# Kernel optimization log

Measured on AMD Instinct MI355X. Metric: run time of the kernel, lower is better.

## Reference

```python
import jax, jax.numpy as jnp
import numpy as np

N_NODES = 50000
N_EDGES = 800000
NFEAT, NHID, NCLASS = 512, 128, 40
PN_SCALE = 1.0


def spmm(edge_row, edge_col, edge_val, h):
    # sparse [N,N] @ dense [N,F]: out[r] += val * h[c] for each edge (r, c)
    msgs = edge_val[:, None] * h[edge_col]  # [E, F]
    return jax.ops.segment_sum(msgs, edge_row, num_segments=N_NODES)


def pair_norm(x):
    # mode 'PN': center columns, scale by mean row norm
    x = x - x.mean(axis=0)
    rownorm_mean = jnp.sqrt(1e-6 + (x * x).sum(axis=1).mean())
    return PN_SCALE * x / rownorm_mean


def setup_inputs() -> dict:
    key = jax.random.key(0)
    ks = jax.random.split(key, 12)

    def uinit(k, shape, fan_out):
        stdv = 1.0 / np.sqrt(fan_out)
        return jax.random.uniform(k, shape, jnp.float32, -stdv, stdv)

    return {
        "x": jax.random.normal(ks[0], (N_NODES, NFEAT), jnp.float32),
        "edge_row": jax.random.randint(ks[1], (N_EDGES,), 0, N_NODES),
        "edge_col": jax.random.randint(ks[2], (N_EDGES,), 0, N_NODES),
        "edge_val": jax.random.uniform(ks[3], (N_EDGES,), jnp.float32),
        "W0": uinit(ks[4], (NFEAT, NHID), NHID),
        "b0": uinit(ks[5], (1, NHID), NHID),
        "W1": uinit(ks[6], (NHID, NHID), NHID),
        "b1": uinit(ks[7], (1, NHID), NHID),
        "W2": uinit(ks[8], (NHID, NHID), NHID),
        "b2": uinit(ks[9], (1, NHID), NHID),
        "W_out": uinit(ks[10], (NHID, NCLASS), NCLASS),
        "b_out": uinit(ks[11], (1, NCLASS), NCLASS),
    }


def reference(x, edge_row, edge_col, edge_val,
              W0, b0, W1, b1, W2, b2, W_out, b_out):
    # DeepGCN forward, eval mode (dropout p=0 is identity), residual=1 -> skip every layer
    x_old = 0.0
    for W, b in ((W0, b0), (W1, b1), (W2, b2)):
        h = x @ W                             # dense mm
        h = spmm(edge_row, edge_col, edge_val, h) + b  # sparse aggregate + bias
        h = pair_norm(h)
        h = jax.nn.relu(h)
        h = h + x_old                         # residual (x_old=0 on first layer)
        x_old = h
        x = h
    out = spmm(edge_row, edge_col, edge_val, x @ W_out) + b_out
    return out
```

## Files before the change

### kernel.cpp

```cpp
#include <hip/hip_runtime.h>
#include <hip/hip_bf16.h>
#include <math.h>

#define N_NODES 50000
#define N_EDGES 800000
#define NFEAT   512
#define NHID    128
#define NCLASS  40
#define NB_STATS 256
#define NPASS    8
#define ROWS_PER_PASS (N_NODES / NPASS)
#define NCB      8
#define CB_W     (N_NODES / NCB)
#define NCNT     (N_NODES * NCB)
#define SCAN_BLOCKS ((NCNT + 1023) / 1024)

typedef short bf16x8 __attribute__((ext_vector_type(8)));
typedef float f32x4  __attribute__((ext_vector_type(4)));

__device__ inline float bf2f(unsigned short u) {
    union { unsigned int i; float f; } x; x.i = ((unsigned int)u) << 16; return x.f;
}

__global__ void hist_kernel(const int* __restrict__ rows, const int* __restrict__ cols,
                            int* __restrict__ cnt, int n) {
    int i = blockIdx.x * blockDim.x + threadIdx.x;
    if (i < n) {
        int r = rows[i];
        int cb = cols[i] / CB_W;
        atomicAdd(&cnt[r * NCB + cb], 1);
    }
}

__global__ __launch_bounds__(1024) void scan_p1_kernel(const int* __restrict__ cnt,
                                                       int* __restrict__ bsum, int n) {
    int i = blockIdx.x * 1024 + threadIdx.x;
    int v = (i < n) ? cnt[i] : 0;
    __shared__ int sm[16];
    int lane = threadIdx.x & 63, w = threadIdx.x >> 6;
    #pragma unroll
    for (int off = 32; off > 0; off >>= 1) v += __shfl_xor(v, off, 64);
    if (lane == 0) sm[w] = v;
    __syncthreads();
    if (threadIdx.x == 0) {
        int s = 0;
        #pragma unroll
        for (int j = 0; j < 16; ++j) s += sm[j];
        bsum[blockIdx.x] = s;
    }
}

__global__ __launch_bounds__(512) void scan_p2_kernel(int* __restrict__ bsum, int nb) {
    __shared__ int wsum[8];
    int t = threadIdx.x;
    int lane = t & 63, w = t >> 6;
    int v = (t < nb) ? bsum[t] : 0;
    int x = v;
    #pragma unroll
    for (int off = 1; off < 64; off <<= 1) {
        int y = __shfl_up(x, off, 64);
        if (lane >= off) x += y;
    }
    if (lane == 63) wsum[w] = x;
    __syncthreads();
    int wbase = 0;
    for (int j = 0; j < w; ++j) wbase += wsum[j];
    if (t < nb) bsum[t] = wbase + x - v;
}

__global__ __launch_bounds__(1024) void scan_p3_kernel(const int* __restrict__ cnt,
                                                       const int* __restrict__ bsum,
                                                       int* __restrict__ bptr,
                                                       int* __restrict__ cursor, int n) {
    __shared__ int wsum[16];
    int b = blockIdx.x;
    int i = b * 1024 + threadIdx.x;
    int lane = threadIdx.x & 63, w = threadIdx.x >> 6;
    int v = (i < n) ? cnt[i] : 0;
    int x = v;
    #pragma unroll
    for (int off = 1; off < 64; off <<= 1) {
        int y = __shfl_up(x, off, 64);
        if (lane >= off) x += y;
    }
    if (lane == 63) wsum[w] = x;
    __syncthreads();
    int wbase = 0;
    for (int j = 0; j < w; ++j) wbase += wsum[j];
    int incl = bsum[b] + wbase + x;
    if (i < n) {
        bptr[i + 1] = incl;
        cursor[i] = incl - v;
    }
    if (i == 0) bptr[0] = 0;
}

__global__ void scatter_kernel(const int* __restrict__ rows, const int* __restrict__ cols,
                               const float* __restrict__ vals, int* __restrict__ cursor,
                               int2* __restrict__ csr_cv, int n, int blocksPerPass) {
    int p = blockIdx.x / blocksPerPass;
    int b = blockIdx.x % blocksPerPass;
    int i = b * 256 + threadIdx.x;
    if (i >= n) return;
    int r = rows[i];
    int lo = p * ROWS_PER_PASS;
    if (r < lo || r >= lo + ROWS_PER_PASS) return;
    int c = cols[i];
    int pos = atomicAdd(&cursor[r * NCB + c / CB_W], 1);
    csr_cv[pos] = make_int2(c, __float_as_int(vals[i]));
}

__global__ __launch_bounds__(256) void wt_cvt_all_kernel(const float* __restrict__ W0,
        const float* __restrict__ W1, const float* __restrict__ W2,
        const float* __restrict__ Wo, __hip_bfloat16* __restrict__ Wt0,
        __hip_bfloat16* __restrict__ Wt1, __hip_bfloat16* __restrict__ Wt2,
        __hip_bfloat16* __restrict__ Wot) {
    int i = blockIdx.x * blockDim.x + threadIdx.x;
    if (i < 65536) {
        int k = i >> 7, n = i & 127;
        Wt0[(size_t)n * 512 + k] = __float2bfloat16(W0[i]);
    } else if (i < 65536 + 16384) {
        int j = i - 65536; int k = j >> 7, n = j & 127;
        Wt1[(size_t)n * 128 + k] = __float2bfloat16(W1[j]);
    } else if (i < 65536 + 32768) {
        int j = i - 65536 - 16384; int k = j >> 7, n = j & 127;
        Wt2[(size_t)n * 128 + k] = __float2bfloat16(W2[j]);
    } else if (i < 65536 + 32768 + 8192) {
        int j = i - 65536 - 32768; int k = j >> 6, n = j & 63;
        float v = (n < NCLASS) ? Wo[k * NCLASS + n] : 0.f;
        Wot[(size_t)n * 128 + k] = __float2bfloat16(v);
    }
}

template<int BM, int BN, int K>
__global__ __launch_bounds__(256) void mfma_gemm(const __hip_bfloat16* __restrict__ Xb,
                                                 const __hip_bfloat16* __restrict__ Wt,
                                                 __hip_bfloat16* __restrict__ Ob, int M) {
    constexpr int BK  = 64;
    constexpr int LDK = 72;
    constexpr int WN  = BN / 64;
    __shared__ short As[BM * LDK];
    __shared__ short Bs[BN * LDK];
    int t = threadIdx.x;
    int lane = t & 63;
    int w = t >> 6;
    int wm = w / WN, wn = w % WN;
    int row0 = blockIdx.x * BM;
    int m0 = wm * 32, n0 = wn * 64;
    int l15 = lane & 15, quad = lane >> 4;

    f32x4 acc[2][4] = {};

    for (int k0 = 0; k0 < K; k0 += BK) {
        #pragma unroll
        for (int idx = t; idx < BM * 8; idx += 256) {
            int r = idx >> 3, c = idx & 7;
            uint4 v = make_uint4(0u, 0u, 0u, 0u);
            if (row0 + r < M)
                v = *(const uint4*)(Xb + (size_t)(row0 + r) * K + k0 + c * 8);
            *(uint4*)(As + r * LDK + c * 8) = v;
        }
        #pragma unroll
        for (int idx = t; idx < BN * 8; idx += 256) {
            int r = idx >> 3, c = idx & 7;
            uint4 v = *(const uint4*)(Wt + (size_t)r * K + k0 + c * 8);
            *(uint4*)(Bs + r * LDK + c * 8) = v;
        }
        __syncthreads();
        #pragma unroll
        for (int ks = 0; ks < 2; ++ks) {
            bf16x8 af[2], bfv[4];
            #pragma unroll
            for (int mt = 0; mt < 2; ++mt)
                af[mt] = *(const bf16x8*)(As + (m0 + mt * 16 + l15) * LDK + ks * 32 + quad * 8);
            #pragma unroll
            for (int nt = 0; nt < 4; ++nt)
                bfv[nt] = *(const bf16x8*)(Bs + (n0 + nt * 16 + l15) * LDK + ks * 32 + quad * 8);
            #pragma unroll
            for (int mt = 0; mt < 2; ++mt)
                #pragma unroll
                for (int nt = 0; nt < 4; ++nt)
                    acc[mt][nt] = __builtin_amdgcn_mfma_f32_16x16x32_bf16(
                        af[mt], bfv[nt], acc[mt][nt], 0, 0, 0);
        }
        __syncthreads();
    }
    #pragma unroll
    for (int mt = 0; mt < 2; ++mt) {
        #pragma unroll
        for (int reg = 0; reg < 4; ++reg) {
            int row = row0 + m0 + mt * 16 + quad * 4 + reg;
            if (row < M) {
                #pragma unroll
                for (int nt = 0; nt < 4; ++nt)
                    Ob[(size_t)row * BN + n0 + nt * 16 + l15] =
                        __float2bfloat16(acc[mt][nt][reg]);
            }
        }
    }
}

template<int BM, int BN, int K>
__global__ __launch_bounds__(256) void mfma_gemm_f32a(const float* __restrict__ Xg,
                                                      const __hip_bfloat16* __restrict__ Wt,
                                                      __hip_bfloat16* __restrict__ Ob, int M) {
    constexpr int BK  = 64;
    constexpr int LDK = 72;
    constexpr int WN  = BN / 64;
    __shared__ short As[BM * LDK];
    __shared__ short Bs[BN * LDK];
    int t = threadIdx.x;
    int lane = t & 63;
    int w = t >> 6;
    int wm = w / WN, wn = w % WN;
    int row0 = blockIdx.x * BM;
    int m0 = wm * 32, n0 = wn * 64;
    int l15 = lane & 15, quad = lane >> 4;

    f32x4 acc[2][4] = {};

    for (int k0 = 0; k0 < K; k0 += BK) {
        #pragma unroll
        for (int idx = t; idx < BM * 16; idx += 256) {
            int r = idx >> 4, c = idx & 15;
            float4 v = make_float4(0.f, 0.f, 0.f, 0.f);
            if (row0 + r < M)
                v = *(const float4*)(Xg + (size_t)(row0 + r) * K + k0 + c * 4);
            __hip_bfloat16 o[4] = {__float2bfloat16(v.x), __float2bfloat16(v.y),
                                   __float2bfloat16(v.z), __float2bfloat16(v.w)};
            *(short4*)(As + r * LDK + c * 4) = *(short4*)o;
        }
        #pragma unroll
        for (int idx = t; idx < BN * 8; idx += 256) {
            int r = idx >> 3, c = idx & 7;
            uint4 v = *(const uint4*)(Wt + (size_t)r * K + k0 + c * 8);
            *(uint4*)(Bs + r * LDK + c * 8) = v;
        }
        __syncthreads();
        #pragma unroll
        for (int ks = 0; ks < 2; ++ks) {
            bf16x8 af[2], bfv[4];
            #pragma unroll
            for (int mt = 0; mt < 2; ++mt)
                af[mt] = *(const bf16x8*)(As + (m0 + mt * 16 + l15) * LDK + ks * 32 + quad * 8);
            #pragma unroll
            for (int nt = 0; nt < 4; ++nt)
                bfv[nt] = *(const bf16x8*)(Bs + (n0 + nt * 16 + l15) * LDK + ks * 32 + quad * 8);
            #pragma unroll
            for (int mt = 0; mt < 2; ++mt)
                #pragma unroll
                for (int nt = 0; nt < 4; ++nt)
                    acc[mt][nt] = __builtin_amdgcn_mfma_f32_16x16x32_bf16(
                        af[mt], bfv[nt], acc[mt][nt], 0, 0, 0);
        }
        __syncthreads();
    }
    #pragma unroll
    for (int mt = 0; mt < 2; ++mt) {
        #pragma unroll
        for (int reg = 0; reg < 4; ++reg) {
            int row = row0 + m0 + mt * 16 + quad * 4 + reg;
            if (row < M) {
                #pragma unroll
                for (int nt = 0; nt < 4; ++nt)
                    Ob[(size_t)row * BN + n0 + nt * 16 + l15] =
                        __float2bfloat16(acc[mt][nt][reg]);
            }
        }
    }
}

__global__ __launch_bounds__(256) void spmm_bf16_kernel(const __hip_bfloat16* __restrict__ H,
                                                        const int* __restrict__ bptr,
                                                        const int2* __restrict__ cv,
                                                        const float* __restrict__ bias,
                                                        __hip_bfloat16* __restrict__ Bm,
                                                        int nrows) {
    int wid = (int)((blockIdx.x * blockDim.x + threadIdx.x) >> 6);
    wid = __builtin_amdgcn_readfirstlane(wid);
    int lane = threadIdx.x & 63;
    int h = lane >> 5;
    int sub = lane & 31;
    if (wid >= nrows) return;
    int s = bptr[wid * NCB];
    int e = bptr[wid * NCB + NCB];
    const ushort4* H4 = (const ushort4*)H;
    f32x4 acc = {0.f, 0.f, 0.f, 0.f};
    int i = s;
    for (; i + 7 < e; i += 8) {
        int2 c0 = cv[i],     c1 = cv[i + 1], c2 = cv[i + 2], c3 = cv[i + 3];
        int2 c4 = cv[i + 4], c5 = cv[i + 5], c6 = cv[i + 6], c7 = cv[i + 7];
        int   ka = h ? c4.x : c0.x;  float va = __int_as_float(h ? c4.y : c0.y);
        int   kb = h ? c5.x : c1.x;  float vb = __int_as_float(h ? c5.y : c1.y);
        int   kc = h ? c6.x : c2.x;  float vc = __int_as_float(h ? c6.y : c2.y);
        int   kd = h ? c7.x : c3.x;  float vd = __int_as_float(h ? c7.y : c3.y);
        ushort4 ga = H4[(size_t)ka * 32 + sub];
        ushort4 gb = H4[(size_t)kb * 32 + sub];
        ushort4 gc = H4[(size_t)kc * 32 + sub];
        ushort4 gd = H4[(size_t)kd * 32 + sub];
        acc[0] = fmaf(va, bf2f(ga.x), acc[0]); acc[1] = fmaf(va, bf2f(ga.y), acc[1]);
        acc[2] = fmaf(va, bf2f(ga.z), acc[2]); acc[3] = fmaf(va, bf2f(ga.w), acc[3]);
        acc[0] = fmaf(vb, bf2f(gb.x), acc[0]); acc[1] = fmaf(vb, bf2f(gb.y), acc[1]);
        acc[2] = fmaf(vb, bf2f(gb.z), acc[2]); acc[3] = fmaf(vb, bf2f(gb.w), acc[3]);
        acc[0] = fmaf(vc, bf2f(gc.x), acc[0]); acc[1] = fmaf(vc, bf2f(gc.y), acc[1]);
        acc[2] = fmaf(vc, bf2f(gc.z), acc[2]); acc[3] = fmaf(vc, bf2f(gc.w), acc[3]);
        acc[0] = fmaf(vd, bf2f(gd.x), acc[0]); acc[1] = fmaf(vd, bf2f(gd.y), acc[1]);
        acc[2] = fmaf(vd, bf2f(gd.z), acc[2]); acc[3] = fmaf(vd, bf2f(gd.w), acc[3]);
    }
    for (; i + 3 < e; i += 4) {
        int2 c0 = cv[i], c1 = cv[i + 1], c2 = cv[i + 2], c3 = cv[i + 3];
        int   ka = h ? c2.x : c0.x;  float va = __int_as_float(h ? c2.y : c0.y);
        int   kb = h ? c3.x : c1.x;  float vb = __int_as_float(h ? c3.y : c1.y);
        ushort4 ga = H4[(size_t)ka * 32 + sub];
        ushort4 gb = H4[(size_t)kb * 32 + sub];
        acc[0] = fmaf(va, bf2f(ga.x), acc[0]); acc[1] = fmaf(va, bf2f(ga.y), acc[1]);
        acc[2] = fmaf(va, bf2f(ga.z), acc[2]); acc[3] = fmaf(va, bf2f(ga.w), acc[3]);
        acc[0] = fmaf(vb, bf2f(gb.x), acc[0]); acc[1] = fmaf(vb, bf2f(gb.y), acc[1]);
        acc[2] = fmaf(vb, bf2f(gb.z), acc[2]); acc[3] = fmaf(vb, bf2f(gb.w), acc[3]);
    }
    for (; i < e; ++i) {
        int2 c = cv[i];
        if (h == 0) {
            float v = __int_as_float(c.y);
            ushort4 g = H4[(size_t)c.x * 32 + sub];
            acc[0] = fmaf(v, bf2f(g.x), acc[0]); acc[1] = fmaf(v, bf2f(g.y), acc[1]);
            acc[2] = fmaf(v, bf2f(g.z), acc[2]); acc[3] = fmaf(v, bf2f(g.w), acc[3]);
        }
    }
    #pragma unroll
    for (int c = 0; c < 4; ++c) acc[c] += __shfl_xor(acc[c], 32);
    if (h == 0) {
        float4 b4 = *(const float4*)(bias + 4 * sub);
        __hip_bfloat16 o[4] = {__float2bfloat16(acc[0] + b4.x), __float2bfloat16(acc[1] + b4.y),
                               __float2bfloat16(acc[2] + b4.z), __float2bfloat16(acc[3] + b4.w)};
        *(ushort4*)(Bm + (size_t)wid * 128 + 4 * sub) = *(ushort4*)o;
    }
}

__global__ __launch_bounds__(256) void stats_kernel(const __hip_bfloat16* __restrict__ B,
                                                    float* __restrict__ partials, int n2) {
    int tid = blockIdx.x * blockDim.x + threadIdx.x;
    int stride = NB_STATS * 256;
    const __hip_bfloat162* B2 = (const __hip_bfloat162*)B;
    float cs0 = 0.f, cs1 = 0.f, sq = 0.f;
    for (int j = tid; j < n2; j += stride) {
        __hip_bfloat162 h = B2[j];
        float a = __bfloat162float(h.x), b = __bfloat162float(h.y);
        cs0 += a; cs1 += b;
        sq = fmaf(a, a, sq); sq = fmaf(b, b, sq);
    }
    __shared__ float s0[256], s1[256], ss[256];
    int t = threadIdx.x;
    s0[t] = cs0; s1[t] = cs1; ss[t] = sq;
    __syncthreads();
    if (t < 64) {
        float a = s0[t] + s0[t + 64] + s0[t + 128] + s0[t + 192];
        float b = s1[t] + s1[t + 64] + s1[t + 128] + s1[t + 192];
        float* pb = partials + (size_t)blockIdx.x * 132;
        pb[2 * t] = a;
        pb[2 * t + 1] = b;
    }
    __syncthreads();
    for (int off = 128; off > 0; off >>= 1) {
        if (t < off) ss[t] += ss[t + off];
        __syncthreads();
    }
    if (t == 0) partials[(size_t)blockIdx.x * 132 + 128] = ss[0];
}

__global__ void finalize_stats_kernel(const float* __restrict__ partials,
                                      float* __restrict__ stats, int nrows) {
    int t = threadIdx.x;
    float cs = 0.f;
    for (int b = 0; b < NB_STATS; ++b) cs += partials[(size_t)b * 132 + t];
    float mu = cs / (float)nrows;
    __shared__ float smu2[128];
    __shared__ float ssq[128];
    float sq = 0.f;
    for (int b = t; b < NB_STATS; b += 128) sq += partials[(size_t)b * 132 + 128];
    smu2[t] = mu * mu;
    ssq[t] = sq;
    __syncthreads();
    for (int off = 64; off > 0; off >>= 1) {
        if (t < off) { smu2[t] += smu2[t + off]; ssq[t] += ssq[t + off]; }
        __syncthreads();
    }
    if (t == 0) {
        float ms = ssq[0] / (float)nrows - smu2[0];
        stats[129] = 1.0f / sqrtf(1e-6f + ms);
    }
    stats[t] = mu;
}

__global__ __launch_bounds__(256) void pn_apply_kernel(const __hip_bfloat16* __restrict__ B,
                                                       const float* __restrict__ stats,
                                                       __hip_bfloat16* __restrict__ Xb,
                                                       int n4, int addResid) {
    int i = blockIdx.x * blockDim.x + threadIdx.x;
    if (i >= n4) return;
    ushort4 bv = *(const ushort4*)(B + (size_t)i * 4);
    __hip_bfloat16* bb = (__hip_bfloat16*)&bv;
    int c4 = (i << 2) & 127;
    float s = stats[129];
    float4 m = ((const float4*)stats)[c4 >> 2];
    float r0 = 0.f, r1 = 0.f, r2 = 0.f, r3 = 0.f;
    if (addResid) {
        ushort4 rv = *(const ushort4*)(Xb + (size_t)i * 4);
        __hip_bfloat16* rb = (__hip_bfloat16*)&rv;
        r0 = __bfloat162float(rb[0]); r1 = __bfloat162float(rb[1]);
        r2 = __bfloat162float(rb[2]); r3 = __bfloat162float(rb[3]);
    }
    __hip_bfloat16 o[4];
    o[0] = __float2bfloat16(fmaxf((__bfloat162float(bb[0]) - m.x) * s, 0.f) + r0);
    o[1] = __float2bfloat16(fmaxf((__bfloat162float(bb[1]) - m.y) * s, 0.f) + r1);
    o[2] = __float2bfloat16(fmaxf((__bfloat162float(bb[2]) - m.z) * s, 0.f) + r2);
    o[3] = __float2bfloat16(fmaxf((__bfloat162float(bb[3]) - m.w) * s, 0.f) + r3);
    *(ushort4*)(Xb + (size_t)i * 4) = *(ushort4*)o;
}

__global__ __launch_bounds__(256) void spmm_out_kernel(const __hip_bfloat16* __restrict__ G,
                                                       const int* __restrict__ bptr,
                                                       const int2* __restrict__ cv,
                                                       const float* __restrict__ bias,
                                                       float* __restrict__ out, int nrows) {
    int wid = (int)((blockIdx.x * blockDim.x + threadIdx.x) >> 6);
    wid = __builtin_amdgcn_readfirstlane(wid);
    int lane = threadIdx.x & 63;
    int h = lane >> 5;
    int sub = lane & 31;
    if (wid >= nrows) return;
    int s = bptr[wid * NCB];
    int e = bptr[wid * NCB + NCB];
    const __hip_bfloat162* G2 = (const __hip_bfloat162*)G;
    float a0 = 0.f, a1 = 0.f;
    int i = s;
    for (; i + 7 < e; i += 8) {
        int2 c0 = cv[i],     c1 = cv[i + 1], c2 = cv[i + 2], c3 = cv[i + 3];
        int2 c4 = cv[i + 4], c5 = cv[i + 5], c6 = cv[i + 6], c7 = cv[i + 7];
        int   ka = h ? c4.x : c0.x;  float va = __int_as_float(h ? c4.y : c0.y);
        int   kb = h ? c5.x : c1.x;  float vb = __int_as_float(h ? c5.y : c1.y);
        int   kc = h ? c6.x : c2.x;  float vc = __int_as_float(h ? c6.y : c2.y);
        int   kd = h ? c7.x : c3.x;  float vd = __int_as_float(h ? c7.y : c3.y);
        __hip_bfloat162 ga = G2[(size_t)ka * 32 + sub];
        __hip_bfloat162 gb = G2[(size_t)kb * 32 + sub];
        __hip_bfloat162 gc = G2[(size_t)kc * 32 + sub];
        __hip_bfloat162 gd = G2[(size_t)kd * 32 + sub];
        a0 = fmaf(va, __bfloat162float(ga.x), a0); a1 = fmaf(va, __bfloat162float(ga.y), a1);
        a0 = fmaf(vb, __bfloat162float(gb.x), a0); a1 = fmaf(vb, __bfloat162float(gb.y), a1);
        a0 = fmaf(vc, __bfloat162float(gc.x), a0); a1 = fmaf(vc, __bfloat162float(gc.y), a1);
        a0 = fmaf(vd, __bfloat162float(gd.x), a0); a1 = fmaf(vd, __bfloat162float(gd.y), a1);
    }
    for (; i + 3 < e; i += 4) {
        int2 c0 = cv[i], c1 = cv[i + 1], c2 = cv[i + 2], c3 = cv[i + 3];
        int   ka = h ? c2.x : c0.x;  float va = __int_as_float(h ? c2.y : c0.y);
        int   kb = h ? c3.x : c1.x;  float vb = __int_as_float(h ? c3.y : c1.y);
        __hip_bfloat162 ga = G2[(size_t)ka * 32 + sub];
        __hip_bfloat162 gb = G2[(size_t)kb * 32 + sub];
        a0 = fmaf(va, __bfloat162float(ga.x), a0); a1 = fmaf(va, __bfloat162float(ga.y), a1);
        a0 = fmaf(vb, __bfloat162float(gb.x), a0); a1 = fmaf(vb, __bfloat162float(gb.y), a1);
    }
    for (; i < e; ++i) {
        int2 c = cv[i];
        if (h == 0) {
            float v = __int_as_float(c.y);
            __hip_bfloat162 g = G2[(size_t)c.x * 32 + sub];
            a0 = fmaf(v, __bfloat162float(g.x), a0);
            a1 = fmaf(v, __bfloat162float(g.y), a1);
        }
    }
    a0 += __shfl_xor(a0, 32);
    a1 += __shfl_xor(a1, 32);
    if (h == 0 && sub < NCLASS / 2) {
        float2 b2 = *(const float2*)(bias + 2 * sub);
        float2 o = make_float2(a0 + b2.x, a1 + b2.y);
        *(float2*)(out + (size_t)wid * NCLASS + 2 * sub) = o;
    }
}

extern "C" void kernel_launch(void* const* d_in, const int* in_sizes, int n_in,
                              void* d_out, int out_size, void* d_ws, size_t ws_size,
                              hipStream_t stream) {
    const float* x        = (const float*)d_in[0];
    const int*   edge_row = (const int*)  d_in[1];
    const int*   edge_col = (const int*)  d_in[2];
    const float* edge_val = (const float*)d_in[3];
    const float* W0 = (const float*)d_in[4];
    const float* b0 = (const float*)d_in[5];
    const float* W1 = (const float*)d_in[6];
    const float* b1 = (const float*)d_in[7];
    const float* W2 = (const float*)d_in[8];
    const float* b2 = (const float*)d_in[9];
    const float* W_out = (const float*)d_in[10];
    const float* b_out = (const float*)d_in[11];
    float* out = (float*)d_out;

    const size_t NH = (size_t)N_NODES * NHID;

    char* p = (char*)d_ws;
    __hip_bfloat16* Xb   = (__hip_bfloat16*)p;  p += NH * 2;
    __hip_bfloat16* A_bf = (__hip_bfloat16*)p;  p += NH * 2;
    __hip_bfloat16* Bm   = (__hip_bfloat16*)p;  p += NH * 2;
    __hip_bfloat16* Wt0 = (__hip_bfloat16*)p;   p += (size_t)128 * 512 * 2;
    __hip_bfloat16* Wt1 = (__hip_bfloat16*)p;   p += (size_t)128 * 128 * 2;
    __hip_bfloat16* Wt2 = (__hip_bfloat16*)p;   p += (size_t)128 * 128 * 2;
    __hip_bfloat16* Wot = (__hip_bfloat16*)p;   p += (size_t)64 * 128 * 2;
    float* stats    = (float*)p;                p += 132 * 4;
    float* partials = (float*)p;                p += (size_t)NB_STATS * 132 * 4;
    int* cnt      = (int*)p;                    p += (size_t)NCNT * 4;
    int* bptr     = (int*)p;                    p += (size_t)(NCNT + 1) * 4 + 4;
    int* cursor   = (int*)p;                    p += (size_t)NCNT * 4;
    int* bsum     = (int*)p;                    p += (size_t)SCAN_BLOCKS * 4 + 4;
    int2* csr_cv  = (int2*)p;                   p += (size_t)N_EDGES * 8;

    const int EB = (N_EDGES + 255) / 256;
    const int SPMM_GRID = (N_NODES + 3) / 4;
    const int PN_GRID = (int)(NH / 4 + 255) / 256;

    wt_cvt_all_kernel<<<(65536 + 32768 + 8192 + 255) / 256, 256, 0, stream>>>(
        W0, W1, W2, W_out, Wt0, Wt1, Wt2, Wot);

    hipMemsetAsync(cnt, 0, NCNT * sizeof(int), stream);
    hist_kernel<<<EB, 256, 0, stream>>>(edge_row, edge_col, cnt, N_EDGES);
    scan_p1_kernel<<<SCAN_BLOCKS, 1024, 0, stream>>>(cnt, bsum, NCNT);
    scan_p2_kernel<<<1, 512, 0, stream>>>(bsum, SCAN_BLOCKS);
    scan_p3_kernel<<<SCAN_BLOCKS, 1024, 0, stream>>>(cnt, bsum, bptr, cursor, NCNT);
    scatter_kernel<<<EB * NPASS, 256, 0, stream>>>(edge_row, edge_col, edge_val, cursor,
                                                   csr_cv, N_EDGES, EB);

    mfma_gemm_f32a<64, 128, 512><<<(N_NODES + 63) / 64, 256, 0, stream>>>(x, Wt0, A_bf, N_NODES);
    spmm_bf16_kernel<<<SPMM_GRID, 256, 0, stream>>>(A_bf, bptr, csr_cv, b0, Bm, N_NODES);
    stats_kernel<<<NB_STATS, 256, 0, stream>>>(Bm, partials, (int)(NH / 2));
    finalize_stats_kernel<<<1, 128, 0, stream>>>(partials, stats, N_NODES);
    pn_apply_kernel<<<PN_GRID, 256, 0, stream>>>(Bm, stats, Xb, (int)(NH / 4), 0);

    const __hip_bfloat16* Wts[2] = {Wt1, Wt2};
    const float* bs[2] = {b1, b2};
    for (int l = 0; l < 2; ++l) {
        mfma_gemm<64, 128, 128><<<(N_NODES + 63) / 64, 256, 0, stream>>>(Xb, Wts[l], A_bf, N_NODES);
        spmm_bf16_kernel<<<SPMM_GRID, 256, 0, stream>>>(A_bf, bptr, csr_cv, bs[l], Bm, N_NODES);
        stats_kernel<<<NB_STATS, 256, 0, stream>>>(Bm, partials, (int)(NH / 2));
        finalize_stats_kernel<<<1, 128, 0, stream>>>(partials, stats, N_NODES);
        pn_apply_kernel<<<PN_GRID, 256, 0, stream>>>(Bm, stats, Xb, (int)(NH / 4), 1);
    }

    mfma_gemm<128, 64, 128><<<(N_NODES + 127) / 128, 256, 0, stream>>>(Xb, Wot, A_bf, N_NODES);
    spmm_out_kernel<<<SPMM_GRID, 256, 0, stream>>>(A_bf, bptr, csr_cv, b_out,
                                                   out, N_NODES);
}
```

Baseline: 496.6 us.

## Fuse PairNorm stats into SpMM and PairNorm apply into next GEMM

Column sums and the sum of squares are now accumulated inside the SpMM kernel: a persistent grid-stride loop reduces into shared memory and then into global stats with atomics. The separate stats, finalize and apply kernels are removed. Normalization, ReLU and the residual add are applied while the next GEMM loads its A tile, and the result is written back to Xb only where later layers need it. This removes several full passes over the hidden activations and many launches, at the cost of global float atomics (non-deterministic summation order) and a persistent SpMM grid that may balance load differently. NPASS for the scatter kernel also changes from 8 to 4.

```diff
diff --git a/kernel.cpp b/kernel.cpp
--- a/kernel.cpp
+++ b/kernel.cpp
@@ -7,13 +7,14 @@
 #define NFEAT   512
 #define NHID    128
 #define NCLASS  40
-#define NB_STATS 256
-#define NPASS    8
+#define NPASS    4
 #define ROWS_PER_PASS (N_NODES / NPASS)
 #define NCB      8
 #define CB_W     (N_NODES / NCB)
 #define NCNT     (N_NODES * NCB)
 #define SCAN_BLOCKS ((NCNT + 1023) / 1024)
+#define NSTAT    132
+#define SPMM_BLOCKS 1024
 
 typedef short bf16x8 __attribute__((ext_vector_type(8)));
 typedef float f32x4  __attribute__((ext_vector_type(4)));
@@ -133,15 +134,17 @@
 }
 
 template<int BM, int BN, int K>
-__global__ __launch_bounds__(256) void mfma_gemm(const __hip_bfloat16* __restrict__ Xb,
-                                                 const __hip_bfloat16* __restrict__ Wt,
-                                                 __hip_bfloat16* __restrict__ Ob, int M) {
+__global__ __launch_bounds__(256) void mfma_gemm_f32a(const float* __restrict__ Xg,
+                                                      const __hip_bfloat16* __restrict__ Wt,
+                                                      __hip_bfloat16* __restrict__ Ob,
+                                                      float* __restrict__ stats_out, int M) {
     constexpr int BK  = 64;
     constexpr int LDK = 72;
     constexpr int WN  = BN / 64;
     __shared__ short As[BM * LDK];
     __shared__ short Bs[BN * LDK];
     int t = threadIdx.x;
+    if (blockIdx.x == 0 && t < NSTAT) stats_out[t] = 0.f;
     int lane = t & 63;
     int w = t >> 6;
     int wm = w / WN, wn = w % WN;
@@ -153,12 +156,14 @@
 
     for (int k0 = 0; k0 < K; k0 += BK) {
         #pragma unroll
-        for (int idx = t; idx < BM * 8; idx += 256) {
-            int r = idx >> 3, c = idx & 7;
-            uint4 v = make_uint4(0u, 0u, 0u, 0u);
+        for (int idx = t; idx < BM * 16; idx += 256) {
+            int r = idx >> 4, c = idx & 15;
+            float4 v = make_float4(0.f, 0.f, 0.f, 0.f);
             if (row0 + r < M)
-                v = *(const uint4*)(Xb + (size_t)(row0 + r) * K + k0 + c * 8);
-            *(uint4*)(As + r * LDK + c * 8) = v;
+                v = *(const float4*)(Xg + (size_t)(row0 + r) * K + k0 + c * 4);
+            __hip_bfloat16 o[4] = {__float2bfloat16(v.x), __float2bfloat16(v.y),
+                                   __float2bfloat16(v.z), __float2bfloat16(v.w)};
+            *(short4*)(As + r * LDK + c * 4) = *(short4*)o;
         }
         #pragma unroll
         for (int idx = t; idx < BN * 8; idx += 256) {
@@ -200,16 +205,39 @@
     }
 }
 
-template<int BM, int BN, int K>
-__global__ __launch_bounds__(256) void mfma_gemm_f32a(const float* __restrict__ Xg,
-                                                      const __hip_bfloat16* __restrict__ Wt,
-                                                      __hip_bfloat16* __restrict__ Ob, int M) {
-    constexpr int BK  = 64;
-    constexpr int LDK = 72;
-    constexpr int WN  = BN / 64;
+template<int BM, int BN, bool ADD_RESID, bool WRITE_X>
+__global__ __launch_bounds__(256) void mfma_gemm_pn(const __hip_bfloat16* __restrict__ Bm,
+                                                    __hip_bfloat16* __restrict__ Xb,
+                                                    const float* __restrict__ stats_in,
+                                                    float* __restrict__ stats_out,
+                                                    const __hip_bfloat16* __restrict__ Wt,
+                                                    __hip_bfloat16* __restrict__ Ob, int M) {
+    constexpr int K = 128, BK = 64, LDK = 72;
+    constexpr int WN = BN / 64;
     __shared__ short As[BM * LDK];
     __shared__ short Bs[BN * LDK];
+    __shared__ float smu[128];
+    __shared__ float sred[128];
+    __shared__ float sscale;
     int t = threadIdx.x;
+    if (stats_out && blockIdx.x == 0 && t < NSTAT) stats_out[t] = 0.f;
+    if (t < 128) {
+        float mu = stats_in[t] * (1.0f / N_NODES);
+        smu[t] = mu;
+        sred[t] = mu * mu;
+    }
+    __syncthreads();
+    for (int off = 64; off > 0; off >>= 1) {
+        if (t < off) sred[t] += sred[t + off];
+        __syncthreads();
+    }
+    if (t == 0) {
+        float ms = stats_in[128] * (1.0f / N_NODES) - sred[0];
+        sscale = 1.0f / sqrtf(1e-6f + ms);
+    }
+    __syncthreads();
+    float sc = sscale;
+
     int lane = t & 63;
     int w = t >> 6;
     int wm = w / WN, wn = w % WN;
@@ -221,14 +249,26 @@
 
     for (int k0 = 0; k0 < K; k0 += BK) {
         #pragma unroll
-        for (int idx = t; idx < BM * 16; idx += 256) {
-            int r = idx >> 4, c = idx & 15;
-            float4 v = make_float4(0.f, 0.f, 0.f, 0.f);
-            if (row0 + r < M)
-                v = *(const float4*)(Xg + (size_t)(row0 + r) * K + k0 + c * 4);
-            __hip_bfloat16 o[4] = {__float2bfloat16(v.x), __float2bfloat16(v.y),
-                                   __float2bfloat16(v.z), __float2bfloat16(v.w)};
-            *(short4*)(As + r * LDK + c * 4) = *(short4*)o;
+        for (int idx = t; idx < BM * 8; idx += 256) {
+            int r = idx >> 3, c = idx & 7;
+            int gr = row0 + r;
+            int k = k0 + c * 8;
+            uint4 bm = make_uint4(0u, 0u, 0u, 0u);
+            uint4 xo = make_uint4(0u, 0u, 0u, 0u);
+            bool ok = gr < M;
+            if (ok) bm = *(const uint4*)(Bm + (size_t)gr * 128 + k);
+            if (ADD_RESID && ok) xo = *(const uint4*)(Xb + (size_t)gr * 128 + k);
+            unsigned short* bu = (unsigned short*)&bm;
+            unsigned short* xu = (unsigned short*)&xo;
+            __hip_bfloat16 o[8];
+            #pragma unroll
+            for (int j = 0; j < 8; ++j) {
+                float v = fmaxf((bf2f(bu[j]) - smu[k + j]) * sc, 0.f);
+                if (ADD_RESID) v += bf2f(xu[j]);
+                o[j] = __float2bfloat16(v);
+            }
+            *(uint4*)(As + r * LDK + c * 8) = *(uint4*)o;
+            if (WRITE_X && ok) *(uint4*)(Xb + (size_t)gr * 128 + k) = *(uint4*)o;
         }
         #pragma unroll
         for (int idx = t; idx < BN * 8; idx += 256) {
@@ -275,147 +315,88 @@
                                                         const int2* __restrict__ cv,
                                                         const float* __restrict__ bias,
                                                         __hip_bfloat16* __restrict__ Bm,
+                                                        float* __restrict__ stats,
                                                         int nrows) {
-    int wid = (int)((blockIdx.x * blockDim.x + threadIdx.x) >> 6);
-    wid = __builtin_amdgcn_readfirstlane(wid);
-    int lane = threadIdx.x & 63;
+    __shared__ float sm[129];
+    int t = threadIdx.x;
+    if (t < 129) sm[t] = 0.f;
+    __syncthreads();
+    int lane = t & 63;
     int h = lane >> 5;
     int sub = lane & 31;
-    if (wid >= nrows) return;
-    int s = bptr[wid * NCB];
-    int e = bptr[wid * NCB + NCB];
+    int wid0 = (int)((blockIdx.x * 256 + t) >> 6);
+    wid0 = __builtin_amdgcn_readfirstlane(wid0);
+    const int NW = SPMM_BLOCKS * 4;
     const ushort4* H4 = (const ushort4*)H;
-    f32x4 acc = {0.f, 0.f, 0.f, 0.f};
-    int i = s;
-    for (; i + 7 < e; i += 8) {
-        int2 c0 = cv[i],     c1 = cv[i + 1], c2 = cv[i + 2], c3 = cv[i + 3];
-        int2 c4 = cv[i + 4], c5 = cv[i + 5], c6 = cv[i + 6], c7 = cv[i + 7];
-        int   ka = h ? c4.x : c0.x;  float va = __int_as_float(h ? c4.y : c0.y);
-        int   kb = h ? c5.x : c1.x;  float vb = __int_as_float(h ? c5.y : c1.y);
-        int   kc = h ? c6.x : c2.x;  float vc = __int_as_float(h ? c6.y : c2.y);
-        int   kd = h ? c7.x : c3.x;  float vd = __int_as_float(h ? c7.y : c3.y);
-        ushort4 ga = H4[(size_t)ka * 32 + sub];
-        ushort4 gb = H4[(size_t)kb * 32 + sub];
-        ushort4 gc = H4[(size_t)kc * 32 + sub];
-        ushort4 gd = H4[(size_t)kd * 32 + sub];
-        acc[0] = fmaf(va, bf2f(ga.x), acc[0]); acc[1] = fmaf(va, bf2f(ga.y), acc[1]);
-        acc[2] = fmaf(va, bf2f(ga.z), acc[2]); acc[3] = fmaf(va, bf2f(ga.w), acc[3]);
-        acc[0] = fmaf(vb, bf2f(gb.x), acc[0]); acc[1] = fmaf(vb, bf2f(gb.y), acc[1]);
-        acc[2] = fmaf(vb, bf2f(gb.z), acc[2]); acc[3] = fmaf(vb, bf2f(gb.w), acc[3]);
-        acc[0] = fmaf(vc, bf2f(gc.x), acc[0]); acc[1] = fmaf(vc, bf2f(gc.y), acc[1]);
-        acc[2] = fmaf(vc, bf2f(gc.z), acc[2]); acc[3] = fmaf(vc, bf2f(gc.w), acc[3]);
-        acc[0] = fmaf(vd, bf2f(gd.x), acc[0]); acc[1] = fmaf(vd, bf2f(gd.y), acc[1]);
-        acc[2] = fmaf(vd, bf2f(gd.z), acc[2]); acc[3] = fmaf(vd, bf2f(gd.w), acc[3]);
-    }
-    for (; i + 3 < e; i += 4) {
-        int2 c0 = cv[i], c1 = cv[i + 1], c2 = cv[i + 2], c3 = cv[i + 3];
-        int   ka = h ? c2.x : c0.x;  float va = __int_as_float(h ? c2.y : c0.y);
-        int   kb = h ? c3.x : c1.x;  float vb = __int_as_float(h ? c3.y : c1.y);
-        ushort4 ga = H4[(size_t)ka * 32 + sub];
-        ushort4 gb = H4[(size_t)kb * 32 + sub];
-        acc[0] = fmaf(va, bf2f(ga.x), acc[0]); acc[1] = fmaf(va, bf2f(ga.y), acc[1]);
-        acc[2] = fmaf(va, bf2f(ga.z), acc[2]); acc[3] = fmaf(va, bf2f(ga.w), acc[3]);
-        acc[0] = fmaf(vb, bf2f(gb.x), acc[0]); acc[1] = fmaf(vb, bf2f(gb.y), acc[1]);
-        acc[2] = fmaf(vb, bf2f(gb.z), acc[2]); acc[3] = fmaf(vb, bf2f(gb.w), acc[3]);
-    }
-    for (; i < e; ++i) {
-        int2 c = cv[i];
+    float4 b4 = *(const float4*)(bias + 4 * sub);
+    f32x4 csum = {0.f, 0.f, 0.f, 0.f};
+    float sq = 0.f;
+
+    for (int wid = wid0; wid < nrows; wid += NW) {
+        int s = bptr[wid * NCB];
+        int e = bptr[wid * NCB + NCB];
+        f32x4 acc = {0.f, 0.f, 0.f, 0.f};
+        int i = s;
+        for (; i + 7 < e; i += 8) {
+            int2 c0 = cv[i],     c1 = cv[i + 1], c2 = cv[i + 2], c3 = cv[i + 3];
+            int2 c4 = cv[i + 4], c5 = cv[i + 5], c6 = cv[i + 6], c7 = cv[i + 7];
+            int   ka = h ? c4.x : c0.x;  float va = __int_as_float(h ? c4.y : c0.y);
+            int   kb = h ? c5.x : c1.x;  float vb = __int_as_float(h ? c5.y : c1.y);
+            int   kc = h ? c6.x : c2.x;  float vc = __int_as_float(h ? c6.y : c2.y);
+            int   kd = h ? c7.x : c3.x;  float vd = __int_as_float(h ? c7.y : c3.y);
+            ushort4 ga = H4[(size_t)ka * 32 + sub];
+            ushort4 gb = H4[(size_t)kb * 32 + sub];
+            ushort4 gc = H4[(size_t)kc * 32 + sub];
+            ushort4 gd = H4[(size_t)kd * 32 + sub];
+            acc[0] = fmaf(va, bf2f(ga.x), acc[0]); acc[1] = fmaf(va, bf2f(ga.y), acc[1]);
+            acc[2] = fmaf(va, bf2f(ga.z), acc[2]); acc[3] = fmaf(va, bf2f(ga.w), acc[3]);
+            acc[0] = fmaf(vb, bf2f(gb.x), acc[0]); acc[1] = fmaf(vb, bf2f(gb.y), acc[1]);
+            acc[2] = fmaf(vb, bf2f(gb.z), acc[2]); acc[3] = fmaf(vb, bf2f(gb.w), acc[3]);
+            acc[0] = fmaf(vc, bf2f(gc.x), acc[0]); acc[1] = fmaf(vc, bf2f(gc.y), acc[1]);
+            acc[2] = fmaf(vc, bf2f(gc.z), acc[2]); acc[3] = fmaf(vc, bf2f(gc.w), acc[3]);
+            acc[0] = fmaf(vd, bf2f(gd.x), acc[0]); acc[1] = fmaf(vd, bf2f(gd.y), acc[1]);
+            acc[2] = fmaf(vd, bf2f(gd.z), acc[2]); acc[3] = fmaf(vd, bf2f(gd.w), acc[3]);
+        }
+        for (; i + 3 < e; i += 4) {
+            int2 c0 = cv[i], c1 = cv[i + 1], c2 = cv[i + 2], c3 = cv[i + 3];
+            int   ka = h ? c2.x : c0.x;  float va = __int_as_float(h ? c2.y : c0.y);
+            int   kb = h ? c3.x : c1.x;  float vb = __int_as_float(h ? c3.y : c1.y);
+            ushort4 ga = H4[(size_t)ka * 32 + sub];
+            ushort4 gb = H4[(size_t)kb * 32 + sub];
+            acc[0] = fmaf(va, bf2f(ga.x), acc[0]); acc[1] = fmaf(va, bf2f(ga.y), acc[1]);
+            acc[2] = fmaf(va, bf2f(ga.z), acc[2]); acc[3] = fmaf(va, bf2f(ga.w), acc[3]);
+            acc[0] = fmaf(vb, bf2f(gb.x), acc[0]); acc[1] = fmaf(vb, bf2f(gb.y), acc[1]);
+            acc[2] = fmaf(vb, bf2f(gb.z), acc[2]); acc[3] = fmaf(vb, bf2f(gb.w), acc[3]);
+        }
+        for (; i < e; ++i) {
+            int2 c = cv[i];
+            if (h == 0) {
+                float v = __int_as_float(c.y);
+                ushort4 g = H4[(size_t)c.x * 32 + sub];
+                acc[0] = fmaf(v, bf2f(g.x), acc[0]); acc[1] = fmaf(v, bf2f(g.y), acc[1]);
+                acc[2] = fmaf(v, bf2f(g.z), acc[2]); acc[3] = fmaf(v, bf2f(g.w), acc[3]);
+            }
+        }
+        #pragma unroll
+        for (int c = 0; c < 4; ++c) acc[c] += __shfl_xor(acc[c], 32);
         if (h == 0) {
-            float v = __int_as_float(c.y);
-            ushort4 g = H4[(size_t)c.x * 32 + sub];
-            acc[0] = fmaf(v, bf2f(g.x), acc[0]); acc[1] = fmaf(v, bf2f(g.y), acc[1]);
-            acc[2] = fmaf(v, bf2f(g.z), acc[2]); acc[3] = fmaf(v, bf2f(g.w), acc[3]);
-        }
-    }
-    #pragma unroll
-    for (int c = 0; c < 4; ++c) acc[c] += __shfl_xor(acc[c], 32);
+            float v0 = acc[0] + b4.x, v1 = acc[1] + b4.y;
+            float v2 = acc[2] + b4.z, v3 = acc[3] + b4.w;
+            __hip_bfloat16 o[4] = {__float2bfloat16(v0), __float2bfloat16(v1),
+                                   __float2bfloat16(v2), __float2bfloat16(v3)};
+            *(ushort4*)(Bm + (size_t)wid * 128 + 4 * sub) = *(ushort4*)o;
+            csum[0] += v0; csum[1] += v1; csum[2] += v2; csum[3] += v3;
+            sq = fmaf(v0, v0, sq); sq = fmaf(v1, v1, sq);
+            sq = fmaf(v2, v2, sq); sq = fmaf(v3, v3, sq);
+        }
+    }
     if (h == 0) {
-        float4 b4 = *(const float4*)(bias + 4 * sub);
-        __hip_bfloat16 o[4] = {__float2bfloat16(acc[0] + b4.x), __float2bfloat16(acc[1] + b4.y),
-                               __float2bfloat16(acc[2] + b4.z), __float2bfloat16(acc[3] + b4.w)};
-        *(ushort4*)(Bm + (size_t)wid * 128 + 4 * sub) = *(ushort4*)o;
-    }
-}
-
-__global__ __launch_bounds__(256) void stats_kernel(const __hip_bfloat16* __restrict__ B,
-                                                    float* __restrict__ partials, int n2) {
-    int tid = blockIdx.x * blockDim.x + threadIdx.x;
-    int stride = NB_STATS * 256;
-    const __hip_bfloat162* B2 = (const __hip_bfloat162*)B;
-    float cs0 = 0.f, cs1 = 0.f, sq = 0.f;
-    for (int j = tid; j < n2; j += stride) {
-        __hip_bfloat162 h = B2[j];
-        float a = __bfloat162float(h.x), b = __bfloat162float(h.y);
-        cs0 += a; cs1 += b;
-        sq = fmaf(a, a, sq); sq = fmaf(b, b, sq);
-    }
-    __shared__ float s0[256], s1[256], ss[256];
-    int t = threadIdx.x;
-    s0[t] = cs0; s1[t] = cs1; ss[t] = sq;
-    __syncthreads();
-    if (t < 64) {
-        float a = s0[t] + s0[t + 64] + s0[t + 128] + s0[t + 192];
-        float b = s1[t] + s1[t + 64] + s1[t + 128] + s1[t + 192];
-        float* pb = partials + (size_t)blockIdx.x * 132;
-        pb[2 * t] = a;
-        pb[2 * t + 1] = b;
-    }
-    __syncthreads();
-    for (int off = 128; off > 0; off >>= 1) {
-        if (t < off) ss[t] += ss[t + off];
-        __syncthreads();
-    }
-    if (t == 0) partials[(size_t)blockIdx.x * 132 + 128] = ss[0];
-}
-
-__global__ void finalize_stats_kernel(const float* __restrict__ partials,
-                                      float* __restrict__ stats, int nrows) {
-    int t = threadIdx.x;
-    float cs = 0.f;
-    for (int b = 0; b < NB_STATS; ++b) cs += partials[(size_t)b * 132 + t];
-    float mu = cs / (float)nrows;
-    __shared__ float smu2[128];
-    __shared__ float ssq[128];
-    float sq = 0.f;
-    for (int b = t; b < NB_STATS; b += 128) sq += partials[(size_t)b * 132 + 128];
-    smu2[t] = mu * mu;
-    ssq[t] = sq;
-    __syncthreads();
-    for (int off = 64; off > 0; off >>= 1) {
-        if (t < off) { smu2[t] += smu2[t + off]; ssq[t] += ssq[t + off]; }
-        __syncthreads();
-    }
-    if (t == 0) {
-        float ms = ssq[0] / (float)nrows - smu2[0];
-        stats[129] = 1.0f / sqrtf(1e-6f + ms);
-    }
-    stats[t] = mu;
-}
-
-__global__ __launch_bounds__(256) void pn_apply_kernel(const __hip_bfloat16* __restrict__ B,
-                                                       const float* __restrict__ stats,
-                                                       __hip_bfloat16* __restrict__ Xb,
-                                                       int n4, int addResid) {
-    int i = blockIdx.x * blockDim.x + threadIdx.x;
-    if (i >= n4) return;
-    ushort4 bv = *(const ushort4*)(B + (size_t)i * 4);
-    __hip_bfloat16* bb = (__hip_bfloat16*)&bv;
-    int c4 = (i << 2) & 127;
-    float s = stats[129];
-    float4 m = ((const float4*)stats)[c4 >> 2];
-    float r0 = 0.f, r1 = 0.f, r2 = 0.f, r3 = 0.f;
-    if (addResid) {
-        ushort4 rv = *(const ushort4*)(Xb + (size_t)i * 4);
-        __hip_bfloat16* rb = (__hip_bfloat16*)&rv;
-        r0 = __bfloat162float(rb[0]); r1 = __bfloat162float(rb[1]);
-        r2 = __bfloat162float(rb[2]); r3 = __bfloat162float(rb[3]);
-    }
-    __hip_bfloat16 o[4];
-    o[0] = __float2bfloat16(fmaxf((__bfloat162float(bb[0]) - m.x) * s, 0.f) + r0);
-    o[1] = __float2bfloat16(fmaxf((__bfloat162float(bb[1]) - m.y) * s, 0.f) + r1);
-    o[2] = __float2bfloat16(fmaxf((__bfloat162float(bb[2]) - m.z) * s, 0.f) + r2);
-    o[3] = __float2bfloat16(fmaxf((__bfloat162float(bb[3]) - m.w) * s, 0.f) + r3);
-    *(ushort4*)(Xb + (size_t)i * 4) = *(ushort4*)o;
+        #pragma unroll
+        for (int j = 0; j < 4; ++j) atomicAdd(&sm[4 * sub + j], csum[j]);
+        atomicAdd(&sm[128], sq);
+    }
+    __syncthreads();
+    if (t < 129) atomicAdd(&stats[t], sm[t]);
 }
 
 __global__ __launch_bounds__(256) void spmm_out_kernel(const __hip_bfloat16* __restrict__ G,
@@ -504,8 +485,8 @@
     __hip_bfloat16* Wt1 = (__hip_bfloat16*)p;   p += (size_t)128 * 128 * 2;
     __hip_bfloat16* Wt2 = (__hip_bfloat16*)p;   p += (size_t)128 * 128 * 2;
     __hip_bfloat16* Wot = (__hip_bfloat16*)p;   p += (size_t)64 * 128 * 2;
-    float* stats    = (float*)p;                p += 132 * 4;
-    float* partials = (float*)p;                p += (size_t)NB_STATS * 132 * 4;
+    float* statsA   = (float*)p;                p += NSTAT * 4;
+    float* statsB   = (float*)p;                p += NSTAT * 4;
     int* cnt      = (int*)p;                    p += (size_t)NCNT * 4;
     int* bptr     = (int*)p;                    p += (size_t)(NCNT + 1) * 4 + 4;
     int* cursor   = (int*)p;                    p += (size_t)NCNT * 4;
@@ -513,8 +494,6 @@
     int2* csr_cv  = (int2*)p;                   p += (size_t)N_EDGES * 8;
 
     const int EB = (N_EDGES + 255) / 256;
-    const int SPMM_GRID = (N_NODES + 3) / 4;
-    const int PN_GRID = (int)(NH / 4 + 255) / 256;
 
     wt_cvt_all_kernel<<<(65536 + 32768 + 8192 + 255) / 256, 256, 0, stream>>>(
         W0, W1, W2, W_out, Wt0, Wt1, Wt2, Wot);
@@ -527,23 +506,23 @@
     scatter_kernel<<<EB * NPASS, 256, 0, stream>>>(edge_row, edge_col, edge_val, cursor,
                                                    csr_cv, N_EDGES, EB);
 
-    mfma_gemm_f32a<64, 128, 512><<<(N_NODES + 63) / 64, 256, 0, stream>>>(x, Wt0, A_bf, N_NODES);
-    spmm_bf16_kernel<<<SPMM_GRID, 256, 0, stream>>>(A_bf, bptr, csr_cv, b0, Bm, N_NODES);
-    stats_kernel<<<NB_STATS, 256, 0, stream>>>(Bm, partials, (int)(NH / 2));
-    finalize_stats_kernel<<<1, 128, 0, stream>>>(partials, stats, N_NODES);
-    pn_apply_kernel<<<PN_GRID, 256, 0, stream>>>(Bm, stats, Xb, (int)(NH / 4), 0);
-
-    const __hip_bfloat16* Wts[2] = {Wt1, Wt2};
-    const float* bs[2] = {b1, b2};
-    for (int l = 0; l < 2; ++l) {
-        mfma_gemm<64, 128, 128><<<(N_NODES + 63) / 64, 256, 0, stream>>>(Xb, Wts[l], A_bf, N_NODES);
-        spmm_bf16_kernel<<<SPMM_GRID, 256, 0, stream>>>(A_bf, bptr, csr_cv, bs[l], Bm, N_NODES);
-        stats_kernel<<<NB_STATS, 256, 0, stream>>>(Bm, partials, (int)(NH / 2));
-        finalize_stats_kernel<<<1, 128, 0, stream>>>(partials, stats, N_NODES);
-        pn_apply_kernel<<<PN_GRID, 256, 0, stream>>>(Bm, stats, Xb, (int)(NH / 4), 1);
-    }
-
-    mfma_gemm<128, 64, 128><<<(N_NODES + 127) / 128, 256, 0, stream>>>(Xb, Wot, A_bf, N_NODES);
-    spmm_out_kernel<<<SPMM_GRID, 256, 0, stream>>>(A_bf, bptr, csr_cv, b_out,
-                                                   out, N_NODES);
-}
+    mfma_gemm_f32a<64, 128, 512><<<(N_NODES + 63) / 64, 256, 0, stream>>>(
+        x, Wt0, A_bf, statsA, N_NODES);
+    spmm_bf16_kernel<<<SPMM_BLOCKS, 256, 0, stream>>>(A_bf, bptr, csr_cv, b0, Bm,
+                                                      statsA, N_NODES);
+
+    mfma_gemm_pn<64, 128, false, true><<<(N_NODES + 63) / 64, 256, 0, stream>>>(
+        Bm, Xb, statsA, statsB, Wt1, A_bf, N_NODES);
+    spmm_bf16_kernel<<<SPMM_BLOCKS, 256, 0, stream>>>(A_bf, bptr, csr_cv, b1, Bm,
+                                                      statsB, N_NODES);
+
+    mfma_gemm_pn<64, 128, true, true><<<(N_NODES + 63) / 64, 256, 0, stream>>>(
+        Bm, Xb, statsB, statsA, Wt2, A_bf, N_NODES);
+    spmm_bf16_kernel<<<SPMM_BLOCKS, 256, 0, stream>>>(A_bf, bptr, csr_cv, b2, Bm,
+                                                      statsA, N_NODES);
+
+    mfma_gemm_pn<128, 64, true, false><<<(N_NODES + 127) / 128, 256, 0, stream>>>(
+        Bm, Xb, statsA, nullptr, Wot, A_bf, N_NODES);
+    spmm_out_kernel<<<(N_NODES + 3) / 4, 256, 0, stream>>>(A_bf, bptr, csr_cv, b_out,
+                                                           out, N_NODES);
+}
```

Measured after the change: 509.4 us. +2.6%, slower.
